# Kernel tuning notes

Measured on AMD Instinct MI355X. Metric: run time of the kernel, lower is better.

## Reference

```python
import jax, jax.numpy as jnp
import numpy as np

# GConvLSTM (torch_geometric_temporal) single step, H=None,C=None -> zeros.
# Each gate g uses two ChebConvs: conv_x_g(X) + conv_h_g(H) + (w_c_g*C for i,f; only i,f,o have w_c) + b_g
# With H=C=0: gate preact = conv_x_g(X) + conv_h_g(0) + b_g. ChebConv(0)=0 only if bias=False;
# torch_geometric_temporal ChebConvs use bias=True by default, so conv_h_g(0) = bias_h_g (a vector).
# We fold conv_h bias into b. Cheb recursion with sym norm, lambda_max=2 default in ChebConv? Actually
# ChebConv requires lambda_max or normalization='sym' default uses lambda_max=2.0 assumption:
# Tx_0 = x; Tx_1 = L_hat @ x where L_hat = -D^-1/2 A D^-1/2 (since L_scaled = L - I = -A_norm for lambda_max=2);
# Tx_k = 2*L_hat@Tx_{k-1} - Tx_{k-2}. out = sum_k Tx_k @ W_k + bias.

MULT = 2
IN_CH = 10
WIDTHS = [8 * MULT, 16 * MULT, 32 * MULT, 76 * MULT]
KS = [2, 3, 4, 5]
NUM_CLASSES = 2
N_NODES = 100000
N_EDGES = 3200000


def _norm_adj(edge_index, n):
    src, dst = edge_index[0], edge_index[1]
    deg = jax.ops.segment_sum(jnp.ones_like(src, dtype=jnp.float32), dst, num_segments=n)
    dinv = jnp.where(deg > 0, jax.lax.rsqrt(jnp.maximum(deg, 1.0)), 0.0)
    w = dinv[src] * dinv[dst]  # [E]
    return src, dst, w


def _lhat_mul(x, src, dst, w, n):
    # L_hat @ x = -A_norm @ x  (lambda_max=2, sym norm, no self loops added in scaled L beyond -I cancel)
    msg = x[src] * w[:, None]  # [E,F]
    agg = jax.ops.segment_sum(msg, dst, num_segments=n)
    return -agg


def cheb_conv(x, Ws, b, src, dst, w, n):
    # Ws: [K, F_in, F_out]
    K = Ws.shape[0]
    Tx0 = x
    out = Tx0 @ Ws[0]
    if K > 1:
        Tx1 = _lhat_mul(Tx0, src, dst, w, n)
        out = out + Tx1 @ Ws[1]
        for k in range(2, K):
            Tx2 = 2.0 * _lhat_mul(Tx1, src, dst, w, n) - Tx0
            out = out + Tx2 @ Ws[k]
            Tx0, Tx1 = Tx1, Tx2
    return out + b


def gconv_lstm_step(x, params, src, dst, w, n):
    # params: dict with per-gate Wx,Wh (cheb weights), bx,bh, b, and w_ci,w_cf,w_co
    def conv_pair(g):
        cx = cheb_conv(x, params[f'Wx_{g}'], params[f'bx_{g}'], src, dst, w, n)
        # H = 0 => conv_h contributes only its bias
        return cx + params[f'bh_{g}'] + params[f'b_{g}']
    # C = 0 => peephole terms w_c*C vanish
    i = jax.nn.sigmoid(conv_pair('i'))
    f = jax.nn.sigmoid(conv_pair('f'))
    c = i * jnp.tanh(conv_pair('c'))
    o = jax.nn.sigmoid(conv_pair('o'))
    h = o * jnp.tanh(c)
    return h


def _make_layer_params(key, f_in, f_out, K):
    p = {}
    ks = jax.random.split(key, 16)
    scale = 1.0 / np.sqrt(f_in * K)
    for gi, g in enumerate(['i', 'f', 'c', 'o']):
        p[f'Wx_{g}'] = jax.random.normal(ks[4 * gi], (K, f_in, f_out), jnp.float32) * scale
        p[f'bx_{g}'] = jnp.zeros((f_out,), jnp.float32)
        p[f'bh_{g}'] = jnp.zeros((f_out,), jnp.float32)
        p[f'b_{g}'] = jnp.zeros((f_out,), jnp.float32)
    return p


def setup_inputs() -> dict:
    key = jax.random.key(0)
    kx, ke, kp, kl = jax.random.split(key, 4)
    x = jax.random.normal(kx, (N_NODES, IN_CH), jnp.float32)
    edge_index = jax.random.randint(ke, (2, N_EDGES), 0, N_NODES, dtype=jnp.int64)
    layer_keys = jax.random.split(kp, 4)
    params = []
    f_in = IN_CH
    for li, (f_out, K) in enumerate(zip(WIDTHS, KS)):
        params.append(_make_layer_params(layer_keys[li], f_in, f_out, K))
        f_in = f_out
    flat = {}
    for li, p in enumerate(params):
        for k, v in p.items():
            flat[f'l{li}_{k}'] = v
    kw, kb = jax.random.split(kl)
    flat['lin_W'] = jax.random.normal(kw, (WIDTHS[-1], NUM_CLASSES), jnp.float32) * (1.0 / np.sqrt(WIDTHS[-1]))
    flat['lin_b'] = jnp.zeros((NUM_CLASSES,), jnp.float32)
    return {'x': x, 'edge_index': edge_index, **flat}


_GATE_KEYS = [f'{pre}_{g}' for g in ['i', 'f', 'c', 'o'] for pre in ['Wx', 'bx', 'bh', 'b']]


def _forward(x, edge_index, params_by_layer, lin_W, lin_b):
    n = x.shape[0]
    src, dst, w = _norm_adj(edge_index, n)
    h = x
    for p in params_by_layer:
        h = gconv_lstm_step(h, p, src, dst, w, n)
        h = jax.nn.relu(h)  # dropout: eval mode -> identity
    logits = h @ lin_W + lin_b
    return jax.nn.softmax(logits, axis=-1)


def reference(x, edge_index,
              l0_Wx_i, l0_bx_i, l0_bh_i, l0_b_i, l0_Wx_f, l0_bx_f, l0_bh_f, l0_b_f, l0_Wx_c, l0_bx_c, l0_bh_c, l0_b_c, l0_Wx_o, l0_bx_o, l0_bh_o, l0_b_o,
              l1_Wx_i, l1_bx_i, l1_bh_i, l1_b_i, l1_Wx_f, l1_bx_f, l1_bh_f, l1_b_f, l1_Wx_c, l1_bx_c, l1_bh_c, l1_b_c, l1_Wx_o, l1_bx_o, l1_bh_o, l1_b_o,
              l2_Wx_i, l2_bx_i, l2_bh_i, l2_b_i, l2_Wx_f, l2_bx_f, l2_bh_f, l2_b_f, l2_Wx_c, l2_bx_c, l2_bh_c, l2_b_c, l2_Wx_o, l2_bx_o, l2_bh_o, l2_b_o,
              l3_Wx_i, l3_bx_i, l3_bh_i, l3_b_i, l3_Wx_f, l3_bx_f, l3_bh_f, l3_b_f, l3_Wx_c, l3_bx_c, l3_bh_c, l3_b_c, l3_Wx_o, l3_bx_o, l3_bh_o, l3_b_o,
              lin_W, lin_b):
    loc = locals()
    params_by_layer = []
    for li in range(4):
        params_by_layer.append({k: loc[f'l{li}_{k}'] for k in _GATE_KEYS})
    return _forward(x, edge_index, params_by_layer, lin_W, lin_b)
```

## Files before the change

### kernel.cpp

```cpp
#include <hip/hip_runtime.h>


#define IN_CH 10
#define PCH 128
#define NB2MAX 512
typedef unsigned short u16;
typedef unsigned long long u64;
typedef short bf16x8 __attribute__((ext_vector_type(8)));
typedef float f32x4 __attribute__((ext_vector_type(4)));

struct __align__(8) Edge { int s; float w; };

__device__ __forceinline__ float bf2f(u16 u) { return __uint_as_float(((unsigned)u) << 16); }
__device__ __forceinline__ float lo16f(unsigned v) { return __uint_as_float(v << 16); }
__device__ __forceinline__ float hi16f(unsigned v) { return __uint_as_float(v & 0xffff0000u); }
__device__ __forceinline__ u16 f2bf(float f) {
    unsigned x = __float_as_uint(f);
    return (u16)((x + 0x7fff + ((x >> 16) & 1)) >> 16);
}
__device__ __forceinline__ float ldv(const float* p) { return *p; }
__device__ __forceinline__ float ldv(const u16* p) { return bf2f(*p); }
__device__ __forceinline__ void stv(float* p, float v) { *p = v; }
__device__ __forceinline__ void stv(u16* p, float v) { *p = f2bf(v); }

__device__ __forceinline__ float ftanh(float x) {
    float t = __expf(2.f * x);
    return 1.f - 2.f / (t + 1.f);
}

__device__ __forceinline__ void gload16(const u16* g, u16* l) {
    __builtin_amdgcn_global_load_lds(
        (const __attribute__((address_space(1))) unsigned*)(const void*)g,
        (__attribute__((address_space(3))) unsigned*)(void*)l, 16, 0, 0);
}


__global__ __launch_bounds__(256) void k_bcount(const int* __restrict__ dst,
                                                int* __restrict__ C, int e, int nb2) {
    __shared__ int sh[NB2MAX];
    const int p = blockIdx.x;
    for (int i = threadIdx.x; i < nb2; i += 256) sh[i] = 0;
    __syncthreads();
    const int chunk = (e + PCH - 1) / PCH;
    const int e0 = p * chunk, e1 = min(e0 + chunk, e);
    for (int i = e0 + threadIdx.x; i < e1; i += 256)
        atomicAdd(&sh[dst[i] >> 8], 1);
    __syncthreads();
    for (int b = threadIdx.x; b < nb2; b += 256) C[b * PCH + p] = sh[b];
}

__global__ __launch_bounds__(512) void k_boff(int* __restrict__ C, int* __restrict__ seg,
                                              int nb2) {
    __shared__ int sh[512];
    const int t = threadIdx.x;
    int tot = 0;
    if (t < nb2) {
        int* Cb = C + (size_t)t * PCH;
        int run = 0;
#pragma unroll 4
        for (int p = 0; p < PCH; p++) { int v = Cb[p]; Cb[p] = run; run += v; }
        tot = run;
    }
    sh[t] = tot;
    __syncthreads();
    for (int off = 1; off < 512; off <<= 1) {
        int x = (t >= off) ? sh[t - off] : 0;
        __syncthreads();
        sh[t] += x;
        __syncthreads();
    }
    const int base = sh[t] - tot;
    if (t < nb2) {
        seg[t] = base;
        int* Cb = C + (size_t)t * PCH;
#pragma unroll 4
        for (int p = 0; p < PCH; p++) Cb[p] += base;
        if (t == nb2 - 1) seg[nb2] = base + tot;
    }
}

__global__ __launch_bounds__(256) void k_stage(const int* __restrict__ src,
                                               const int* __restrict__ dst,
                                               const int* __restrict__ C,
                                               int* __restrict__ Sd, int* __restrict__ Ss,
                                               int e, int nb2) {
    __shared__ int cur[NB2MAX];
    const int p = blockIdx.x;
    for (int i = threadIdx.x; i < nb2; i += 256) cur[i] = C[(size_t)i * PCH + p];
    __syncthreads();
    const int chunk = (e + PCH - 1) / PCH;
    const int e0 = p * chunk, e1 = min(e0 + chunk, e);
    for (int i = e0 + threadIdx.x; i < e1; i += 256) {
        int d = dst[i], s = src[i];
        int pos = atomicAdd(&cur[d >> 8], 1);
        Sd[pos] = d;
        Ss[pos] = s;
    }
}

__global__ __launch_bounds__(256) void k_bknt(const int* __restrict__ Sd,
                                              const int* __restrict__ seg,
                                              int* __restrict__ cnt, int n) {
    __shared__ int sh[256];
    const int b = blockIdx.x;
    sh[threadIdx.x] = 0;
    __syncthreads();
    const int lo = seg[b], hi = seg[b + 1];
    for (int i = lo + threadIdx.x; i < hi; i += 256)
        atomicAdd(&sh[Sd[i] & 255], 1);
    __syncthreads();
    int node = b * 256 + threadIdx.x;
    if (node < n) cnt[node] = sh[threadIdx.x];
}

__global__ __launch_bounds__(256) void k_bscat(const int* __restrict__ Sd,
                                               const int* __restrict__ Ss,
                                               const int* __restrict__ seg,
                                               const int* __restrict__ row_ptr,
                                               const float* __restrict__ dinv,
                                               Edge* __restrict__ ed, int n) {
    __shared__ int cur[256];
    const int b = blockIdx.x;
    int node = b * 256 + threadIdx.x;
    cur[threadIdx.x] = node < n ? row_ptr[node] : 0;
    __syncthreads();
    const int lo = seg[b], hi = seg[b + 1];
    for (int i = lo + threadIdx.x; i < hi; i += 256) {
        int d = Sd[i], s = Ss[i];
        int pos = atomicAdd(&cur[d & 255], 1);
        float w = dinv[s] * dinv[d];
        u64 v = (u64)(unsigned)s | ((u64)__float_as_uint(w) << 32);
        *(u64*)&ed[pos] = v;
    }
}

__global__ void k_dinv(const int* __restrict__ cnt, float* __restrict__ dinv, int n) {
    int i = blockIdx.x * 256 + threadIdx.x;
    if (i < n) dinv[i] = cnt[i] > 0 ? rsqrtf((float)cnt[i]) : 0.f;
}


__global__ void k_bsum(const int* __restrict__ cnt, int* __restrict__ bsum, int n) {
    __shared__ int red[256];
    int t = threadIdx.x;
    int idx = blockIdx.x * 1024 + t * 4;
    int s = 0;
#pragma unroll
    for (int j = 0; j < 4; j++) s += (idx + j < n) ? cnt[idx + j] : 0;
    red[t] = s;
    __syncthreads();
    for (int off = 128; off > 0; off >>= 1) {
        if (t < off) red[t] += red[t + off];
        __syncthreads();
    }
    if (t == 0) bsum[blockIdx.x] = red[0];
}

__global__ __launch_bounds__(1024) void k_bscan(const int* __restrict__ bsum,
                                                int* __restrict__ boff,
                                                int* __restrict__ total_out, int B) {
    __shared__ int sh[1024];
    int t = threadIdx.x;
    int v = t < B ? bsum[t] : 0;
    sh[t] = v;
    __syncthreads();
    for (int off = 1; off < 1024; off <<= 1) {
        int x = (t >= off) ? sh[t - off] : 0;
        __syncthreads();
        sh[t] += x;
        __syncthreads();
    }
    if (t < B) boff[t] = sh[t] - v;
    if (t == B - 1) *total_out = sh[t];
}

__global__ void k_write(const int* __restrict__ cnt, const int* __restrict__ boff,
                        int* __restrict__ row_ptr, int* __restrict__ cursor, int n) {
    __shared__ int tsum[256];
    int t = threadIdx.x;
    int idx = blockIdx.x * 1024 + t * 4;
    int c[4];
    int s = 0;
#pragma unroll
    for (int j = 0; j < 4; j++) {
        c[j] = (idx + j < n) ? cnt[idx + j] : 0;
        s += c[j];
    }
    tsum[t] = s;
    __syncthreads();
    for (int off = 1; off < 256; off <<= 1) {
        int x = (t >= off) ? tsum[t - off] : 0;
        __syncthreads();
        tsum[t] += x;
        __syncthreads();
    }
    int run = boff[blockIdx.x] + tsum[t] - s;
#pragma unroll
    for (int j = 0; j < 4; j++) {
        if (idx + j < n) {
            row_ptr[idx + j] = run;
            cursor[idx + j] = run;
            run += c[j];
        }
    }
}


template <int F>
__global__ void k_spmv(const u16* __restrict__ X, const u16* __restrict__ Tprev,
                       u16* __restrict__ Tout, const int* __restrict__ row_ptr,
                       const Edge* __restrict__ ed, int n, float scale) {
    int lane = threadIdx.x;
    int node = blockIdx.x * blockDim.y + threadIdx.y;
    if (node >= n) return;
    int lo = row_ptr[node], hi = row_ptr[node + 1];
    const u16* Xc = X + 2 * lane;
    float a0[4] = {0.f, 0.f, 0.f, 0.f};
    float a1[4] = {0.f, 0.f, 0.f, 0.f};
    int e = lo;
    for (; e + 8 <= hi; e += 8) {
        Edge q[8];
#pragma unroll
        for (int j = 0; j < 8; j++) q[j] = ed[e + j];
        unsigned v[8];
#pragma unroll
        for (int j = 0; j < 8; j++)
            v[j] = *(const unsigned*)(Xc + (size_t)q[j].s * F);
#pragma unroll
        for (int j = 0; j < 8; j++) {
            a0[j & 3] = fmaf(q[j].w, lo16f(v[j]), a0[j & 3]);
            a1[j & 3] = fmaf(q[j].w, hi16f(v[j]), a1[j & 3]);
        }
    }
    for (; e + 4 <= hi; e += 4) {
        Edge q[4];
#pragma unroll
        for (int j = 0; j < 4; j++) q[j] = ed[e + j];
        unsigned v[4];
#pragma unroll
        for (int j = 0; j < 4; j++)
            v[j] = *(const unsigned*)(Xc + (size_t)q[j].s * F);
#pragma unroll
        for (int j = 0; j < 4; j++) {
            a0[j] = fmaf(q[j].w, lo16f(v[j]), a0[j]);
            a1[j] = fmaf(q[j].w, hi16f(v[j]), a1[j]);
        }
    }
    for (; e < hi; e++) {
        Edge q = ed[e];
        unsigned v = *(const unsigned*)(Xc + (size_t)q.s * F);
        a0[0] = fmaf(q.w, lo16f(v), a0[0]);
        a1[0] = fmaf(q.w, hi16f(v), a1[0]);
    }
    float v0 = -scale * ((a0[0] + a0[1]) + (a0[2] + a0[3]));
    float v1 = -scale * ((a1[0] + a1[1]) + (a1[2] + a1[3]));
    if (Tprev) {
        unsigned pv = *(const unsigned*)(Tprev + (size_t)node * F + 2 * lane);
        v0 -= lo16f(pv);
        v1 -= hi16f(pv);
    }
    *(unsigned*)(Tout + (size_t)node * F + 2 * lane) =
        (unsigned)f2bf(v0) | ((unsigned)f2bf(v1) << 16);
}

struct TP { const void* p[5]; };

template <typename ST, int FIN, int K>
__global__ __launch_bounds__(256) void k_chebgate(TP tp, const float* __restrict__ Wp,
                                                  const float* __restrict__ b4,
                                                  ST* __restrict__ H, int n, int F,
                                                  int F4pad) {
    __shared__ float As[FIN][68];
    __shared__ float Ws[FIN][128];
    const int tid = threadIdx.x;
    const int fx = tid & 31, ry = tid >> 5;
    const int row0 = blockIdx.y * 64;
    const int f0 = blockIdx.x * 32;
    const int f = f0 + fx;

    float acc[8][3];
    const float4 bv = *(const float4*)&b4[(size_t)f * 4];
#pragma unroll
    for (int r = 0; r < 8; r++) { acc[r][0] = bv.x; acc[r][1] = bv.y; acc[r][2] = bv.z; }

#pragma unroll
    for (int t = 0; t < K; t++) {
        const ST* T = (const ST*)tp.p[t];
        for (int idx = tid; idx < 64 * FIN; idx += 256) {
            int r = idx / FIN, a = idx - r * FIN;
            int rr = row0 + r;
            if (rr >= n) rr = n - 1;
            As[a][r] = ldv(&T[(size_t)rr * FIN + a]);
        }
        const float* Wt = Wp + (size_t)t * FIN * F4pad + (size_t)f0 * 4;
        for (int idx = tid; idx < FIN * 128; idx += 256) {
            int aa = idx >> 7, c = idx & 127;
            Ws[aa][c] = Wt[(size_t)aa * F4pad + c];
        }
        __syncthreads();
#pragma unroll 2
        for (int a = 0; a < FIN; a++) {
            const float4 w = *(const float4*)&Ws[a][fx * 4];
            const float4 x0 = *(const float4*)&As[a][ry * 8];
            const float4 x1 = *(const float4*)&As[a][ry * 8 + 4];
            const float xr[8] = {x0.x, x0.y, x0.z, x0.w, x1.x, x1.y, x1.z, x1.w};
#pragma unroll
            for (int r = 0; r < 8; r++) {
                acc[r][0] = fmaf(xr[r], w.x, acc[r][0]);
                acc[r][1] = fmaf(xr[r], w.y, acc[r][1]);
                acc[r][2] = fmaf(xr[r], w.z, acc[r][2]);
            }
        }
        __syncthreads();
    }

    if (f < F) {
#pragma unroll
        for (int r = 0; r < 8; r++) {
            int row = row0 + ry * 8 + r;
            if (row < n) {
                float gi = 1.f / (1.f + __expf(-acc[r][0]));
                float go = 1.f / (1.f + __expf(-acc[r][2]));
                float c = gi * ftanh(acc[r][1]);
                float h = go * ftanh(c);
                stv(&H[(size_t)row * F + f], fmaxf(h, 0.f));
            }
        }
    }
}


template <int FIN, int K, int NT, int FPAD>
__global__ __launch_bounds__(256) void k_chebgate_mfma2(TP tp, const u16* __restrict__ Bp,
                                                        const float* __restrict__ b3,
                                                        u16* __restrict__ H, int n, int F,
                                                        int Hstride) {
    constexpr int NIT = K * FIN / 32;
    constexpr int CPR = FIN / 8;
    constexpr int CSH = (CPR == 8) ? 3 : 2;
    constexpr int PANEL = 128 * FIN;
    constexpr int IPT = (128 * CPR) / 256;
    __shared__ __align__(16) u16 Alds[K * PANEL];

    const int tid = threadIdx.x;
    const int xb = blockIdx.x;
    const int wv = tid >> 6, lane = tid & 63;
    const int ln = lane & 15, lk = lane >> 4;
    const size_t panel_g = (size_t)xb * 128 * FIN;

#pragma unroll
    for (int t = 0; t < K; t++) {
        const u16* g = (const u16*)tp.p[t] + panel_g;
#pragma unroll
        for (int i = 0; i < IPT; i++) {
            int j0 = wv * (IPT * 64) + i * 64;
            int j = j0 + lane;
            int row = j >> CSH, c = j & (CPR - 1);
            int sc = (j & ~(CPR - 1)) | (c ^ (row & (CPR - 1)));
            gload16(g + (size_t)sc * 8, Alds + (size_t)t * PANEL + (size_t)j0 * 8);
        }
    }
    __syncthreads();

    const int r0 = xb * 128 + wv * 32;
    const u16* Bl = Bp + (size_t)lane * 8;

#pragma unroll 1
    for (int yb = 0; yb < NT; yb++) {
        f32x4 acc[2][2][3];
#pragma unroll
        for (int rt = 0; rt < 2; rt++)
#pragma unroll
            for (int s = 0; s < 2; s++)
#pragma unroll
                for (int g = 0; g < 3; g++) acc[rt][s][g] = (f32x4){0.f, 0.f, 0.f, 0.f};

#pragma unroll
        for (int it = 0; it < NIT; it++) {
            const int k0 = it * 32;
            const int t = k0 / FIN;
            const int a0 = k0 % FIN;
            bf16x8 af[2];
#pragma unroll
            for (int rt = 0; rt < 2; rt++) {
                int lrow = wv * 32 + rt * 16 + ln;
                int kc = (a0 >> 3) + lk;
                int kcs = kc ^ (lrow & (CPR - 1));
                af[rt] = *(const bf16x8*)(Alds + (size_t)t * PANEL + (size_t)lrow * FIN + kcs * 8);
            }
#pragma unroll
            for (int s = 0; s < 2; s++)
#pragma unroll
                for (int g = 0; g < 3; g++) {
                    int fi = (yb * NIT + it) * 6 + s * 3 + g;
                    bf16x8 bf = *(const bf16x8*)(Bl + (size_t)fi * 512);
#pragma unroll
                    for (int rt = 0; rt < 2; rt++)
                        acc[rt][s][g] = __builtin_amdgcn_mfma_f32_16x16x32_bf16(
                            af[rt], bf, acc[rt][s][g], 0, 0, 0);
                }
        }

        const int f0 = yb * 32;
#pragma unroll
        for (int s = 0; s < 2; s++) {
            int fcol = f0 + s * 16 + ln;
            if (fcol >= F) continue;
            float bi = b3[0 * FPAD + fcol];
            float bc = b3[1 * FPAD + fcol];
            float bo = b3[2 * FPAD + fcol];
#pragma unroll
            for (int rt = 0; rt < 2; rt++) {
#pragma unroll
                for (int reg = 0; reg < 4; reg++) {
                    int row = r0 + rt * 16 + lk * 4 + reg;
                    if (row < n) {
                        float gi = 1.f / (1.f + __expf(-(acc[rt][s][0][reg] + bi)));
                        float go = 1.f / (1.f + __expf(-(acc[rt][s][2][reg] + bo)));
                        float c = gi * ftanh(acc[rt][s][1][reg] + bc);
                        float h = go * ftanh(c);
                        H[(size_t)row * Hstride + fcol] = f2bf(fmaxf(h, 0.f));
                    }
                }
            }
        }
    }
}


template <int FIN, int K, int NT, int FPAD>
__global__ __launch_bounds__(512, 4) void k_chebgate_mfma_fused2(
    TP tp, const u16* __restrict__ Bp, const float* __restrict__ b3,
    const float* __restrict__ W2, float* __restrict__ part, int n, int F) {
    constexpr int NIT = K * FIN / 32;
    constexpr int CPR = FIN / 8;
    constexpr int CSH = (CPR == 8) ? 3 : 2;
    constexpr int PANEL = 128 * FIN;
    constexpr int IPT = (128 * CPR) / 512;
    __shared__ __align__(16) u16 Alds[K * PANEL];

    const int tid = threadIdx.x;
    const int xb = blockIdx.x;
    const int wv = tid >> 6, lane = tid & 63;
    const int ln = lane & 15, lk = lane >> 4;
    const size_t panel_g = (size_t)xb * 128 * FIN;

#pragma unroll
    for (int t = 0; t < K; t++) {
        const u16* g = (const u16*)tp.p[t] + panel_g;
#pragma unroll
        for (int i = 0; i < IPT; i++) {
            int j0 = wv * (IPT * 64) + i * 64;
            int j = j0 + lane;
            int row = j >> CSH, c = j & (CPR - 1);
            int sc = (j & ~(CPR - 1)) | (c ^ (row & (CPR - 1)));
            gload16(g + (size_t)sc * 8, Alds + (size_t)t * PANEL + (size_t)j0 * 8);
        }
    }
    __syncthreads();

    const int r0 = xb * 128 + wv * 16;
    const int lrow = wv * 16 + ln;
    const int rmask = lrow & (CPR - 1);
    const u16* Bl = Bp + (size_t)lane * 8;

#pragma unroll 1
    for (int yb = 0; yb < NT; yb++) {
        f32x4 acc[2][3];
#pragma unroll
        for (int s = 0; s < 2; s++)
#pragma unroll
            for (int g = 0; g < 3; g++) acc[s][g] = (f32x4){0.f, 0.f, 0.f, 0.f};

#pragma unroll
        for (int it = 0; it < NIT; it++) {
            const int k0 = it * 32;
            const int t = k0 / FIN;
            const int a0 = k0 % FIN;
            int kcs = ((a0 >> 3) + lk) ^ rmask;
            bf16x8 af = *(const bf16x8*)(Alds + (size_t)t * PANEL + (size_t)lrow * FIN + kcs * 8);
#pragma unroll
            for (int s = 0; s < 2; s++)
#pragma unroll
                for (int g = 0; g < 3; g++) {
                    int fi = (yb * NIT + it) * 6 + s * 3 + g;
                    bf16x8 bf = *(const bf16x8*)(Bl + (size_t)fi * 512);
                    acc[s][g] = __builtin_amdgcn_mfma_f32_16x16x32_bf16(
                        af, bf, acc[s][g], 0, 0, 0);
                }
        }

        const int f0 = yb * 32;
        float p0[4], p1[4];
#pragma unroll
        for (int reg = 0; reg < 4; reg++) { p0[reg] = 0.f; p1[reg] = 0.f; }

#pragma unroll
        for (int s = 0; s < 2; s++) {
            int fcol = f0 + s * 16 + ln;
            float w20 = fcol < F ? W2[fcol * 2 + 0] : 0.f;
            float w21 = fcol < F ? W2[fcol * 2 + 1] : 0.f;
            float bi = b3[0 * FPAD + fcol];
            float bc = b3[1 * FPAD + fcol];
            float bo = b3[2 * FPAD + fcol];
#pragma unroll
            for (int reg = 0; reg < 4; reg++) {
                float gi = 1.f / (1.f + __expf(-(acc[s][0][reg] + bi)));
                float go = 1.f / (1.f + __expf(-(acc[s][2][reg] + bo)));
                float c = gi * ftanh(acc[s][1][reg] + bc);
                float h = fmaxf(go * ftanh(c), 0.f);
                p0[reg] = fmaf(h, w20, p0[reg]);
                p1[reg] = fmaf(h, w21, p1[reg]);
            }
        }

#pragma unroll
        for (int reg = 0; reg < 4; reg++) {
            float v0 = p0[reg], v1 = p1[reg];
#pragma unroll
            for (int m = 1; m <= 8; m <<= 1) {
                v0 += __shfl_xor(v0, m);
                v1 += __shfl_xor(v1, m);
            }
            p0[reg] = v0;
            p1[reg] = v1;
        }

        if (ln == 0) {
#pragma unroll
            for (int reg = 0; reg < 4; reg++) {
                int row = r0 + lk * 4 + reg;
                if (row < n) {
                    float* pp = part + ((size_t)yb * n + row) * 2;
                    pp[0] = p0[reg];
                    pp[1] = p1[reg];
                }
            }
        }
    }
}

__global__ void k_smax(const float* __restrict__ part, const float* __restrict__ b,
                       float* __restrict__ out, int n, int ntiles) {
    int i = blockIdx.x * 256 + threadIdx.x;
    if (i >= n) return;
    float l0 = b[0], l1 = b[1];
    for (int t = 0; t < ntiles; t++) {
        const float* pp = part + ((size_t)t * n + i) * 2;
        l0 += pp[0];
        l1 += pp[1];
    }
    float m = fmaxf(l0, l1);
    float e0 = __expf(l0 - m), e1 = __expf(l1 - m);
    float s = 1.f / (e0 + e1);
    out[(size_t)i * 2 + 0] = e0 * s;
    out[(size_t)i * 2 + 1] = e1 * s;
}


__global__ void k_pack_w(const float* __restrict__ Wi, const float* __restrict__ Wc,
                         const float* __restrict__ Wo, float* __restrict__ Wp,
                         int KFIN, int F, int F4pad) {
    int idx = blockIdx.x * 256 + threadIdx.x;
    int tot = KFIN * F4pad;
    if (idx >= tot) return;
    int c = idx % F4pad;
    int ka = idx / F4pad;
    int f = c >> 2, g = c & 3;
    float v = 0.f;
    if (g < 3 && f < F) {
        const float* Wg = (g == 0) ? Wi : ((g == 1) ? Wc : Wo);
        v = Wg[(size_t)ka * F + f];
    }
    Wp[idx] = v;
}

__global__ void k_pack_b(const float* __restrict__ bxi, const float* __restrict__ bhi,
                         const float* __restrict__ bi, const float* __restrict__ bxc,
                         const float* __restrict__ bhc, const float* __restrict__ bc,
                         const float* __restrict__ bxo, const float* __restrict__ bho,
                         const float* __restrict__ bo, float* __restrict__ b4,
                         int F, int F4pad) {
    int idx = blockIdx.x * 256 + threadIdx.x;
    if (idx >= F4pad) return;
    int f = idx >> 2, g = idx & 3;
    float v = 0.f;
    if (g < 3 && f < F) {
        if (g == 0) v = bxi[f] + bhi[f] + bi[f];
        else if (g == 1) v = bxc[f] + bhc[f] + bc[f];
        else v = bxo[f] + bho[f] + bo[f];
    }
    b4[idx] = v;
}

__global__ void k_pack_wf(const float* __restrict__ Wi, const float* __restrict__ Wc,
                          const float* __restrict__ Wo, u16* __restrict__ Bp,
                          int NIT, int Fin, int F, int NT) {
    int idx = blockIdx.x * 256 + threadIdx.x;
    int tot = NT * NIT * 6 * 512;
    if (idx >= tot) return;
    int frag = idx >> 9;
    int r = idx & 511;
    int lane = r >> 3, j = r & 7;
    int lk = lane >> 4, ln = lane & 15;
    int yb = frag / (NIT * 6);
    int q = frag % (NIT * 6);
    int it = q / 6, sg = q % 6;
    int s = sg / 3, g = sg % 3;
    int fcol = yb * 32 + s * 16 + ln;
    int k = it * 32 + lk * 8 + j;
    int t = k / Fin, a = k % Fin;
    float v = 0.f;
    if (fcol < F) {
        const float* Wg = (g == 0) ? Wi : ((g == 1) ? Wc : Wo);
        v = Wg[((size_t)t * Fin + a) * F + fcol];
    }
    Bp[idx] = f2bf(v);
}

__global__ void k_pack_b3(const float* __restrict__ bxi, const float* __restrict__ bhi,
                          const float* __restrict__ bi, const float* __restrict__ bxc,
                          const float* __restrict__ bhc, const float* __restrict__ bc,
                          const float* __restrict__ bxo, const float* __restrict__ bho,
                          const float* __restrict__ bo, float* __restrict__ b3,
                          int F, int FPAD) {
    int idx = blockIdx.x * 256 + threadIdx.x;
    if (idx >= 3 * FPAD) return;
    int g = idx / FPAD, f = idx % FPAD;
    float v = 0.f;
    if (f < F) {
        if (g == 0) v = bxi[f] + bhi[f] + bi[f];
        else if (g == 1) v = bxc[f] + bhc[f] + bc[f];
        else v = bxo[f] + bho[f] + bo[f];
    }
    b3[idx] = v;
}

__global__ void k_cvt(const float* __restrict__ x, u16* __restrict__ y, int n) {
    int i = blockIdx.x * 256 + threadIdx.x;
    if (i < n) y[i] = f2bf(x[i]);
}


static inline size_t al(size_t x) { return (x + 255) & ~(size_t)255; }

extern "C" void kernel_launch(void* const* d_in, const int* in_sizes, int n_in,
                              void* d_out, int out_size, void* d_ws, size_t ws_size,
                              hipStream_t stream) {
    const float* X0 = (const float*)d_in[0];
    const int* ei = (const int*)d_in[1];
    const int N = in_sizes[0] / IN_CH;
    const int E = in_sizes[1] / 2;
    const int* src = ei;
    const int* dst = ei + E;

    char* p = (char*)d_ws;
    size_t off = 0;
    auto carve = [&](size_t bytes) -> char* { char* r = p + off; off += al(bytes); return r; };
    int* row_ptr  = (int*)carve((size_t)(N + 1) * 4);
    int* cnt      = (int*)carve((size_t)N * 4);
    int* cursor   = (int*)carve((size_t)N * 4);
    float* dinv   = (float*)carve((size_t)N * 4);
    int* bsum     = (int*)carve((size_t)1024 * 4);
    int* boff     = (int*)carve((size_t)1024 * 4);
    int* Cb       = (int*)carve((size_t)NB2MAX * PCH * 4);
    int* seg      = (int*)carve((size_t)(NB2MAX + 1) * 4);
    Edge* edges   = (Edge*)carve((size_t)E * 8);
    const size_t S64 = al((size_t)N * 64 * 2);
    char* bufA    = carve(5 * S64);
    char* bufB    = carve((size_t)N * 304);
    float* Wp     = (float*)carve((size_t)48 * 128 * 4);
    float* b4     = (float*)carve((size_t)128 * 4);
    u16* Wt       = (u16*)carve((size_t)480 * 320 * 2);
    float* b3     = (float*)carve((size_t)480 * 4);
    (void)ws_size;

    u16* X0c  = (u16*)bufA;
    u16* T0_1 = (u16*)(bufA + al((size_t)N * 20));
    u16* H0   = (u16*)(bufA + S64);
    u16* T1_1 = (u16*)(bufA + S64 + al((size_t)N * 32));
    u16* T1_2 = (u16*)(bufA + S64 + 2 * al((size_t)N * 32));
    u16* L2T[4];
    for (int t = 0; t < 4; t++) L2T[t] = (u16*)(bufB + t * al((size_t)N * 64));
    u16* L3T[5];
    for (int t = 0; t < 5; t++) L3T[t] = (u16*)(bufA + t * S64);
    float* part = (float*)bufB;
    int* Sd = (int*)bufA;
    int* Ss = (int*)(bufA + al((size_t)E * 4));

    int gN = (N + 255) / 256;
    int B = (N + 1023) / 1024;
    int nb2 = (N + 255) / 256;
    k_bcount<<<PCH, 256, 0, stream>>>(dst, Cb, E, nb2);
    k_boff<<<1, 512, 0, stream>>>(Cb, seg, nb2);
    k_stage<<<PCH, 256, 0, stream>>>(src, dst, Cb, Sd, Ss, E, nb2);
    k_bknt<<<nb2, 256, 0, stream>>>(Sd, seg, cnt, N);
    k_dinv<<<gN, 256, 0, stream>>>(cnt, dinv, N);
    k_bsum<<<B, 256, 0, stream>>>(cnt, bsum, N);
    k_bscan<<<1, 1024, 0, stream>>>(bsum, boff, row_ptr + N, B);
    k_write<<<B, 256, 0, stream>>>(cnt, boff, row_ptr, cursor, N);
    k_bscat<<<nb2, 256, 0, stream>>>(Sd, Ss, seg, row_ptr, dinv, edges, N);

    k_cvt<<<(N * IN_CH + 255) / 256, 256, 0, stream>>>(X0, X0c, N * IN_CH);

    dim3 gv(1, (N + 63) / 64);
    int rb = (N + 127) / 128;

    dim3 bs5(5, 48);   int g5 = (N + 47) / 48;
    dim3 bs8(8, 32);   int g8 = (N + 31) / 32;
    dim3 bs16(16, 16); int g16 = (N + 15) / 16;
    dim3 bs32(32, 8);  int g32 = (N + 7) / 8;

    {
        k_pack_w<<<(20 * 128 + 255) / 256, 256, 0, stream>>>(
            (const float*)d_in[2], (const float*)d_in[10], (const float*)d_in[14], Wp, 20, 16, 128);
        k_pack_b<<<1, 256, 0, stream>>>(
            (const float*)d_in[3], (const float*)d_in[4], (const float*)d_in[5],
            (const float*)d_in[11], (const float*)d_in[12], (const float*)d_in[13],
            (const float*)d_in[15], (const float*)d_in[16], (const float*)d_in[17], b4, 16, 128);
        k_spmv<10><<<g5, bs5, 0, stream>>>(X0c, nullptr, T0_1, row_ptr, edges, N, 1.f);
        TP tp; tp.p[0] = X0c; tp.p[1] = T0_1;
        k_chebgate<u16, 10, 2><<<gv, 256, 0, stream>>>(tp, Wp, b4, H0, N, 16, 128);
    }
    {
        k_pack_w<<<(48 * 128 + 255) / 256, 256, 0, stream>>>(
            (const float*)d_in[18], (const float*)d_in[26], (const float*)d_in[30], Wp, 48, 32, 128);
        k_pack_b<<<1, 256, 0, stream>>>(
            (const float*)d_in[19], (const float*)d_in[20], (const float*)d_in[21],
            (const float*)d_in[27], (const float*)d_in[28], (const float*)d_in[29],
            (const float*)d_in[31], (const float*)d_in[32], (const float*)d_in[33], b4, 32, 128);
        k_spmv<16><<<g8, bs8, 0, stream>>>(H0, nullptr, T1_1, row_ptr, edges, N, 1.f);
        k_spmv<16><<<g8, bs8, 0, stream>>>(T1_1, H0, T1_2, row_ptr, edges, N, 2.f);
        TP tp; tp.p[0] = H0; tp.p[1] = T1_1; tp.p[2] = T1_2;
        k_chebgate<u16, 16, 3><<<gv, 256, 0, stream>>>(tp, Wp, b4, L2T[0], N, 32, 128);
    }
    {
        k_pack_wf<<<(2 * 4 * 6 * 512 + 255) / 256, 256, 0, stream>>>(
            (const float*)d_in[34], (const float*)d_in[42], (const float*)d_in[46], Wt, 4, 32, 64, 2);
        k_pack_b3<<<1, 256, 0, stream>>>(
            (const float*)d_in[35], (const float*)d_in[36], (const float*)d_in[37],
            (const float*)d_in[43], (const float*)d_in[44], (const float*)d_in[45],
            (const float*)d_in[47], (const float*)d_in[48], (const float*)d_in[49], b3, 64, 64);
        k_spmv<32><<<g16, bs16, 0, stream>>>(L2T[0], nullptr, L2T[1], row_ptr, edges, N, 1.f);
        k_spmv<32><<<g16, bs16, 0, stream>>>(L2T[1], L2T[0], L2T[2], row_ptr, edges, N, 2.f);
        k_spmv<32><<<g16, bs16, 0, stream>>>(L2T[2], L2T[1], L2T[3], row_ptr, edges, N, 2.f);
        TP tp; for (int t = 0; t < 4; t++) tp.p[t] = L2T[t];
        k_chebgate_mfma2<32, 4, 2, 64><<<rb, 256, 0, stream>>>(tp, Wt, b3, L3T[0], N, 64, 64);
    }
    {
        k_pack_wf<<<(5 * 10 * 6 * 512 + 255) / 256, 256, 0, stream>>>(
            (const float*)d_in[50], (const float*)d_in[58], (const float*)d_in[62], Wt, 10, 64, 152, 5);
        k_pack_b3<<<2, 256, 0, stream>>>(
            (const float*)d_in[51], (const float*)d_in[52], (const float*)d_in[53],
            (const float*)d_in[59], (const float*)d_in[60], (const float*)d_in[61],
            (const float*)d_in[63], (const float*)d_in[64], (const float*)d_in[65], b3, 152, 160);
        k_spmv<64><<<g32, bs32, 0, stream>>>(L3T[0], nullptr, L3T[1], row_ptr, edges, N, 1.f);
        k_spmv<64><<<g32, bs32, 0, stream>>>(L3T[1], L3T[0], L3T[2], row_ptr, edges, N, 2.f);
        k_spmv<64><<<g32, bs32, 0, stream>>>(L3T[2], L3T[1], L3T[3], row_ptr, edges, N, 2.f);
        k_spmv<64><<<g32, bs32, 0, stream>>>(L3T[3], L3T[2], L3T[4], row_ptr, edges, N, 2.f);
        TP tp; for (int t = 0; t < 5; t++) tp.p[t] = L3T[t];
        k_chebgate_mfma_fused2<64, 5, 5, 160><<<rb, 512, 0, stream>>>(
            tp, Wt, b3, (const float*)d_in[66], part, N, 152);
    }

    k_smax<<<gN, 256, 0, stream>>>(part, (const float*)d_in[67], (float*)d_out, N, 5);
}
```

Baseline: 1.028 ms.

## Double-buffer packed B weights in LDS and shrink fused gate tile to 64 rows

The final-layer fused Cheb-gate kernel moves from 128-row/512-thread blocks to 64-row/256-thread blocks. Its nested yb/it loop is flattened into one loop over weight chunks. Each chunk of packed B weights is staged into a double-buffered LDS region with async loads, overlapping the next chunk's load with the current MFMAs. This replaces per-lane global B reads with LDS reads and shrinks the A panel, but adds a __syncthreads per iteration and launches twice as many blocks, each reloading the full weight stream.

Result: slower. 1.060 ms (+3.1%).

```diff
diff --git a/kernel.cpp b/kernel.cpp
--- a/kernel.cpp
+++ b/kernel.cpp
@@ -429,21 +429,23 @@
 
 
 template <int FIN, int K, int NT, int FPAD>
-__global__ __launch_bounds__(512, 4) void k_chebgate_mfma_fused2(
+__global__ __launch_bounds__(256) void k_chebgate_mfma_fused2(
     TP tp, const u16* __restrict__ Bp, const float* __restrict__ b3,
     const float* __restrict__ W2, float* __restrict__ part, int n, int F) {
     constexpr int NIT = K * FIN / 32;
+    constexpr int NQ = NT * NIT;
     constexpr int CPR = FIN / 8;
     constexpr int CSH = (CPR == 8) ? 3 : 2;
-    constexpr int PANEL = 128 * FIN;
-    constexpr int IPT = (128 * CPR) / 512;
+    constexpr int PANEL = 64 * FIN;
+    constexpr int IPT = (64 * CPR) / 256;
     __shared__ __align__(16) u16 Alds[K * PANEL];
+    __shared__ __align__(16) u16 Blds[2 * 6 * 512];
 
     const int tid = threadIdx.x;
     const int xb = blockIdx.x;
     const int wv = tid >> 6, lane = tid & 63;
     const int ln = lane & 15, lk = lane >> 4;
-    const size_t panel_g = (size_t)xb * 128 * FIN;
+    const size_t panel_g = (size_t)xb * 64 * FIN;
 
 #pragma unroll
     for (int t = 0; t < K; t++) {
@@ -457,86 +459,100 @@
             gload16(g + (size_t)sc * 8, Alds + (size_t)t * PANEL + (size_t)j0 * 8);
         }
     }
-    __syncthreads();
-
-    const int r0 = xb * 128 + wv * 16;
+
+    auto stageB = [&](int buf, int q) {
+        if (q < NQ) {
+            for (int f = wv; f < 6; f += 4)
+                gload16(Bp + (((size_t)q * 6 + f) << 9) + lane * 8,
+                        Blds + buf * 3072 + f * 512);
+        }
+    };
+    stageB(0, 0);
+    __syncthreads();
+
+    const int r0 = xb * 64 + wv * 16;
     const int lrow = wv * 16 + ln;
     const int rmask = lrow & (CPR - 1);
-    const u16* Bl = Bp + (size_t)lane * 8;
-
+
+    f32x4 acc[2][3];
+#pragma unroll
+    for (int s = 0; s < 2; s++)
+#pragma unroll
+        for (int g = 0; g < 3; g++) acc[s][g] = (f32x4){0.f, 0.f, 0.f, 0.f};
+
+    int buf = 0;
 #pragma unroll 1
-    for (int yb = 0; yb < NT; yb++) {
-        f32x4 acc[2][3];
+    for (int q = 0; q < NQ; q++) {
+        const int it = q % NIT;
+        stageB(buf ^ 1, q + 1);
+        const int k0 = it * 32;
+        const int t = k0 / FIN;
+        const int a0 = k0 % FIN;
+        int kcs = ((a0 >> 3) + lk) ^ rmask;
+        bf16x8 af = *(const bf16x8*)(Alds + (size_t)t * PANEL + (size_t)lrow * FIN + kcs * 8);
+        const u16* Bq = Blds + buf * 3072;
 #pragma unroll
         for (int s = 0; s < 2; s++)
 #pragma unroll
-            for (int g = 0; g < 3; g++) acc[s][g] = (f32x4){0.f, 0.f, 0.f, 0.f};
-
-#pragma unroll
-        for (int it = 0; it < NIT; it++) {
-            const int k0 = it * 32;
-            const int t = k0 / FIN;
-            const int a0 = k0 % FIN;
-            int kcs = ((a0 >> 3) + lk) ^ rmask;
-            bf16x8 af = *(const bf16x8*)(Alds + (size_t)t * PANEL + (size_t)lrow * FIN + kcs * 8);
-#pragma unroll
-            for (int s = 0; s < 2; s++)
-#pragma unroll
-                for (int g = 0; g < 3; g++) {
-                    int fi = (yb * NIT + it) * 6 + s * 3 + g;
-                    bf16x8 bf = *(const bf16x8*)(Bl + (size_t)fi * 512);
-                    acc[s][g] = __builtin_amdgcn_mfma_f32_16x16x32_bf16(
-                        af, bf, acc[s][g], 0, 0, 0);
-                }
-        }
-
-        const int f0 = yb * 32;
-        float p0[4], p1[4];
-#pragma unroll
-        for (int reg = 0; reg < 4; reg++) { p0[reg] = 0.f; p1[reg] = 0.f; }
-
-#pragma unroll
-        for (int s = 0; s < 2; s++) {
-            int fcol = f0 + s * 16 + ln;
-            float w20 = fcol < F ? W2[fcol * 2 + 0] : 0.f;
-            float w21 = fcol < F ? W2[fcol * 2 + 1] : 0.f;
-            float bi = b3[0 * FPAD + fcol];
-            float bc = b3[1 * FPAD + fcol];
-            float bo = b3[2 * FPAD + fcol];
-#pragma unroll
-            for (int reg = 0; reg < 4; reg++) {
-                float gi = 1.f / (1.f + __expf(-(acc[s][0][reg] + bi)));
-                float go = 1.f / (1.f + __expf(-(acc[s][2][reg] + bo)));
-                float c = gi * ftanh(acc[s][1][reg] + bc);
-                float h = fmaxf(go * ftanh(c), 0.f);
-                p0[reg] = fmaf(h, w20, p0[reg]);
-                p1[reg] = fmaf(h, w21, p1[reg]);
+            for (int g = 0; g < 3; g++) {
+                bf16x8 bf = *(const bf16x8*)(Bq + (s * 3 + g) * 512 + (size_t)lane * 8);
+                acc[s][g] = __builtin_amdgcn_mfma_f32_16x16x32_bf16(af, bf, acc[s][g], 0, 0, 0);
             }
-        }
-
-#pragma unroll
-        for (int reg = 0; reg < 4; reg++) {
-            float v0 = p0[reg], v1 = p1[reg];
-#pragma unroll
-            for (int m = 1; m <= 8; m <<= 1) {
-                v0 += __shfl_xor(v0, m);
-                v1 += __shfl_xor(v1, m);
-            }
-            p0[reg] = v0;
-            p1[reg] = v1;
-        }
-
-        if (ln == 0) {
-#pragma unroll
-            for (int reg = 0; reg < 4; reg++) {
-                int row = r0 + lk * 4 + reg;
-                if (row < n) {
-                    float* pp = part + ((size_t)yb * n + row) * 2;
-                    pp[0] = p0[reg];
-                    pp[1] = p1[reg];
+
+        if (it == NIT - 1) {
+            const int yb = q / NIT;
+            const int f0 = yb * 32;
+            float p0[4], p1[4];
+#pragma unroll
+            for (int reg = 0; reg < 4; reg++) { p0[reg] = 0.f; p1[reg] = 0.f; }
+#pragma unroll
+            for (int s = 0; s < 2; s++) {
+                int fcol = f0 + s * 16 + ln;
+                float w20 = fcol < F ? W2[fcol * 2 + 0] : 0.f;
+                float w21 = fcol < F ? W2[fcol * 2 + 1] : 0.f;
+                float bi = b3[0 * FPAD + fcol];
+                float bc = b3[1 * FPAD + fcol];
+                float bo = b3[2 * FPAD + fcol];
+#pragma unroll
+                for (int reg = 0; reg < 4; reg++) {
+                    float gi = 1.f / (1.f + __expf(-(acc[s][0][reg] + bi)));
+                    float go = 1.f / (1.f + __expf(-(acc[s][2][reg] + bo)));
+                    float c = gi * ftanh(acc[s][1][reg] + bc);
+                    float h = fmaxf(go * ftanh(c), 0.f);
+                    p0[reg] = fmaf(h, w20, p0[reg]);
+                    p1[reg] = fmaf(h, w21, p1[reg]);
                 }
             }
-        }
+#pragma unroll
+            for (int reg = 0; reg < 4; reg++) {
+                float v0 = p0[reg], v1 = p1[reg];
+#pragma unroll
+                for (int m = 1; m <= 8; m <<= 1) {
+                    v0 += __shfl_xor(v0, m);
+                    v1 += __shfl_xor(v1, m);
+                }
+                p0[reg] = v0;
+                p1[reg] = v1;
+            }
+            if (ln == 0) {
+#pragma unroll
+                for (int reg = 0; reg < 4; reg++) {
+                    int row = r0 + lk * 4 + reg;
+                    if (row < n) {
+                        float* pp = part + ((size_t)yb * n + row) * 2;
+                        pp[0] = p0[reg];
+                        pp[1] = p1[reg];
+                    }
+                }
+            }
+#pragma unroll
+            for (int s = 0; s < 2; s++)
+#pragma unroll
+                for (int g = 0; g < 3; g++) acc[s][g] = (f32x4){0.f, 0.f, 0.f, 0.f};
+        }
+
+        __syncthreads();
+        buf ^= 1;
     }
 }
 
@@ -705,6 +721,7 @@
 
     dim3 gv(1, (N + 63) / 64);
     int rb = (N + 127) / 128;
+    int rb64 = (N + 63) / 64;
 
     dim3 bs5(5, 48);   int g5 = (N + 47) / 48;
     dim3 bs8(8, 32);   int g8 = (N + 31) / 32;
@@ -759,7 +776,7 @@
         k_spmv<64><<<g32, bs32, 0, stream>>>(L3T[2], L3T[1], L3T[3], row_ptr, edges, N, 2.f);
         k_spmv<64><<<g32, bs32, 0, stream>>>(L3T[3], L3T[2], L3T[4], row_ptr, edges, N, 2.f);
         TP tp; for (int t = 0; t < 5; t++) tp.p[t] = L3T[t];
-        k_chebgate_mfma_fused2<64, 5, 5, 160><<<rb, 512, 0, stream>>>(
+        k_chebgate_mfma_fused2<64, 5, 5, 160><<<rb64, 256, 0, stream>>>(
             tp, Wt, b3, (const float*)d_in[66], part, N, 152);
     }
 
```
